# Kernel tuning notes

Hardware: AMD Instinct MI355X
Metric: run time of the kernel (lower is better)

The kernel has to match this reference:

```python
import jax, jax.numpy as jnp
import numpy as np

N_INST, N_PERS, N_PROD = 20000, 50000, 30000
E_INST, E_PERS, E_PROD = 160000, 400000, 240000
F_IN, HID, HEADS, OUT = 128, 64, 4, 2
D = HID * HEADS  # 256
NEG_SLOPE_ATT = 0.2   # GATv2 attention leaky-relu slope
NEG_SLOPE_ACT = 0.01  # F.leaky_relu default
BN_EPS = 1e-5


def gatv2(x, src, dst, Wl, Wr, att, b, N):
    """Single-relation GATv2Conv (concat heads, add_self_loops=True)."""
    loop = jnp.arange(N, dtype=src.dtype)
    s = jnp.concatenate([src, loop])
    d = jnp.concatenate([dst, loop])
    H, C = att.shape
    hl = (x @ Wl).reshape(N, H, C)  # source transform
    hr = (x @ Wr).reshape(N, H, C)  # target transform
    e = jax.nn.leaky_relu(hl[s] + hr[d], NEG_SLOPE_ATT)        # [E,H,C]
    score = jnp.einsum('ehc,hc->eh', e, att)                   # [E,H]
    mx = jax.lax.stop_gradient(jax.ops.segment_max(score, d, num_segments=N))
    ex = jnp.exp(score - mx[d])
    den = jax.ops.segment_sum(ex, d, num_segments=N)           # [N,H]
    alpha = ex / (den[d] + 1e-16)
    out = jax.ops.segment_sum(alpha[..., None] * hl[s], d, num_segments=N)
    return out.reshape(N, H * C) + b


def batchnorm(x, g, b):
    mu = jnp.mean(x, axis=0)
    var = jnp.var(x, axis=0)
    return (x - mu) * jax.lax.rsqrt(var + BN_EPS) * g + b


def setup_inputs() -> dict:
    key = jax.random.key(0)
    ks = jax.random.split(key, 16)
    s = 0.05
    return {
        'x_inst': jax.random.normal(ks[0], (N_INST, F_IN), jnp.float32),
        'x_pers': jax.random.normal(ks[1], (N_PERS, F_IN), jnp.float32),
        'x_prod': jax.random.normal(ks[2], (N_PROD, F_IN), jnp.float32),
        'ei_inst': jax.random.randint(ks[3], (2, E_INST), 0, N_INST, jnp.int32),
        'ei_pers': jax.random.randint(ks[4], (2, E_PERS), 0, N_PERS, jnp.int32),
        'ei_prod': jax.random.randint(ks[5], (2, E_PROD), 0, N_PROD, jnp.int32),
        'Wl1': jax.random.normal(ks[6], (3, F_IN, D), jnp.float32) * s,
        'Wr1': jax.random.normal(ks[7], (3, F_IN, D), jnp.float32) * s,
        'att1': jax.random.normal(ks[8], (3, HEADS, HID), jnp.float32) * s,
        'b1': jnp.zeros((3, D), jnp.float32),
        'Wl2': jax.random.normal(ks[9], (3, D, D), jnp.float32) * s,
        'Wr2': jax.random.normal(ks[10], (3, D, D), jnp.float32) * s,
        'att2': jax.random.normal(ks[11], (3, HEADS, HID), jnp.float32) * s,
        'b2': jnp.zeros((3, D), jnp.float32),
        'bn_g': jnp.ones((3, D), jnp.float32),
        'bn_b': jnp.zeros((3, D), jnp.float32),
        'cW': jax.random.normal(ks[12], (D, OUT), jnp.float32) * s,
        'cb': jnp.zeros((OUT,), jnp.float32),
    }


def reference(x_inst, x_pers, x_prod, ei_inst, ei_pers, ei_prod,
              Wl1, Wr1, att1, b1, Wl2, Wr2, att2, b2,
              bn_g, bn_b, cW, cb):
    xs = (x_inst, x_pers, x_prod)
    eis = (ei_inst, ei_pers, ei_prod)
    outs = []
    for i in range(3):  # fixed set of node types
        x = xs[i]
        N = x.shape[0]
        src, dst = eis[i][0], eis[i][1]
        h = gatv2(x, src, dst, Wl1[i], Wr1[i], att1[i], b1[i], N)
        h = jax.nn.leaky_relu(batchnorm(h, bn_g[i], bn_b[i]), NEG_SLOPE_ACT)
        h = gatv2(h, src, dst, Wl2[i], Wr2[i], att2[i], b2[i], N)
        h = jax.nn.leaky_relu(batchnorm(h, bn_g[i], bn_b[i]), NEG_SLOPE_ACT)
        outs.append(h @ cW + cb)
    return tuple(outs)
```

## Files before the change

### kernel.cpp

```cpp
#include <hip/hip_runtime.h>

#define DFEAT 256
#define NEG_ATT 0.2f
#define NEG_ACT 0.01f
#define BN_EPS 1e-5f

typedef short bf16x8 __attribute__((ext_vector_type(8)));
typedef float f32x4 __attribute__((ext_vector_type(4)));

struct Int3 { int a[3]; };
struct Cp3 { const void* p[3]; };
struct Vp3 { void* p[3]; };

__device__ __forceinline__ float lrelu(float x, float s) { return x > 0.f ? x : s * x; }

__device__ __forceinline__ unsigned short f2bf(float f) {
    union { float f; unsigned int u; } v; v.f = f;
    unsigned int u = v.u;
    unsigned int r = (u + 0x7FFFu + ((u >> 16) & 1u)) >> 16;
    return (unsigned short)r;
}
__device__ __forceinline__ float bf2f(unsigned short s) {
    union { unsigned int u; float f; } v; v.u = ((unsigned int)s) << 16;
    return v.f;
}

__global__ __launch_bounds__(256)
void hist_all_k(Cp3 dst, Int3 E, int* __restrict__ counts_all, Int3 nodeOff) {
    int t = blockIdx.y;
    int e = blockIdx.x * 256 + threadIdx.x;
    if (e >= E.a[t]) return;
    const int* dstp = (const int*)dst.p[t];
    atomicAdd(&counts_all[nodeOff.a[t] + dstp[e]], 1);
}

__global__ __launch_bounds__(256)
void scan1_all_k(const int* __restrict__ counts_all, int* __restrict__ offs_all,
                 int* __restrict__ bsums_all, Int3 N, Int3 nodeOff, Int3 bOff) {
    int t = blockIdx.y;
    if (blockIdx.x * 256 >= N.a[t]) return;
    const int* counts = counts_all + nodeOff.a[t];
    int* offs = offs_all + nodeOff.a[t] + t;
    int* bsums = bsums_all + bOff.a[t];
    __shared__ int buf[256];
    int tt = threadIdx.x;
    int i = blockIdx.x * 256 + tt;
    int v = (i < N.a[t]) ? counts[i] : 0;
    buf[tt] = v;
    __syncthreads();
    for (int off = 1; off < 256; off <<= 1) {
        int x = (tt >= off) ? buf[tt - off] : 0;
        __syncthreads();
        buf[tt] += x;
        __syncthreads();
    }
    if (i < N.a[t]) offs[i] = buf[tt];
    if (tt == 255) bsums[blockIdx.x] = buf[255];
}

__global__ __launch_bounds__(256)
void scan2_all_k(int* __restrict__ bsums_all, Int3 N, Int3 bOff) {
    int t = blockIdx.x;
    int nb = (N.a[t] + 255) / 256;
    int* bsums = bsums_all + bOff.a[t];
    __shared__ int buf[256];
    __shared__ int carry_s;
    int tt = threadIdx.x;
    if (tt == 0) carry_s = 0;
    __syncthreads();
    for (int base = 0; base < nb; base += 256) {
        int i = base + tt;
        int v = (i < nb) ? bsums[i] : 0;
        buf[tt] = v;
        __syncthreads();
        for (int off = 1; off < 256; off <<= 1) {
            int x = (tt >= off) ? buf[tt - off] : 0;
            __syncthreads();
            buf[tt] += x;
            __syncthreads();
        }
        int incl = buf[tt];
        int c = carry_s;
        if (i < nb) bsums[i] = c + incl - v;
        __syncthreads();
        if (tt == 255) carry_s = c + buf[255];
        __syncthreads();
    }
}

__global__ __launch_bounds__(256)
void scan3_all_k(int* __restrict__ offs_all, const int* __restrict__ counts_all,
                 const int* __restrict__ bsums_all, Int3 N, Int3 E,
                 Int3 nodeOff, Int3 bOff) {
    int t = blockIdx.y;
    if (blockIdx.x * 256 >= N.a[t]) return;
    int* offs = offs_all + nodeOff.a[t] + t;
    const int* counts = counts_all + nodeOff.a[t];
    const int* bsums = bsums_all + bOff.a[t];
    int i = blockIdx.x * 256 + threadIdx.x;
    if (i < N.a[t]) offs[i] = offs[i] - counts[i] + bsums[blockIdx.x];
    if (i == 0) offs[N.a[t]] = E.a[t];
}

__global__ __launch_bounds__(256)
void scatter_all_k(Cp3 src, Cp3 dst, Int3 E, const int* __restrict__ offs_all,
                   int* __restrict__ counts_all, int* __restrict__ csr_all,
                   Int3 nodeOff, Int3 edgeOff) {
    int t = blockIdx.y;
    int e = blockIdx.x * 256 + threadIdx.x;
    if (e >= E.a[t]) return;
    const int* srcp = (const int*)src.p[t];
    const int* dstp = (const int*)dst.p[t];
    const int* offs = offs_all + nodeOff.a[t] + t;
    int* cursor = counts_all + nodeOff.a[t];
    int* csr = csr_all + edgeOff.a[t];
    int d = dstp[e];
    int pos = atomicSub(&cursor[d], 1) - 1;
    csr[offs[d] + pos] = srcp[e];
}

__global__ __launch_bounds__(256)
void wcast_all_k(const float* __restrict__ Wl1, const float* __restrict__ Wr1,
                 const float* __restrict__ Wl2, const float* __restrict__ Wr2,
                 unsigned short* __restrict__ Bt1, unsigned short* __restrict__ Bt2) {
    int idx = blockIdx.x * 256 + threadIdx.x;
    const int S1 = 3 * 512 * 128;
    const int S2 = 3 * 512 * 256;
    if (idx < S1) {
        int ty = idx / (512 * 128);
        int r = idx - ty * (512 * 128);
        int n = r >> 7, k = r & 127;
        const float* W = ((n < 256) ? Wl1 : Wr1) + (size_t)ty * 128 * 256;
        Bt1[idx] = f2bf(W[(size_t)k * 256 + (n & 255)]);
    } else if (idx < S1 + S2) {
        int r2 = idx - S1;
        int ty = r2 / (512 * 256);
        int r = r2 - ty * (512 * 256);
        int n = r >> 8, k = r & 255;
        const float* W = ((n < 256) ? Wl2 : Wr2) + (size_t)ty * 256 * 256;
        Bt2[r2] = f2bf(W[(size_t)k * 256 + (n & 255)]);
    }
}

template<int AF32>
__global__ __launch_bounds__(256)
void mfma_gemm_all_k(Cp3 Ap3, Cp3 Bp3, Vp3 Cp3v, Int3 M3, int K) {
    int t = blockIdx.z;
    int M = M3.a[t];
    int bm = blockIdx.x * 128;
    if (bm >= M) return;
    const void* Ap = Ap3.p[t];
    const unsigned short* Bt = (const unsigned short*)Bp3.p[t];
    unsigned short* C = (unsigned short*)Cp3v.p[t];
    const int LDK = 40;
    __shared__ unsigned short As[128 * LDK];
    __shared__ unsigned short Bs[128 * LDK];
    int tid = threadIdx.x;
    int bn = blockIdx.y * 128;
    int wid = tid >> 6, lane = tid & 63;
    int quad = lane >> 4, l16 = lane & 15;
    int mw = (wid & 1) * 64, nw = (wid >> 1) * 64;
    f32x4 acc[4][4] = {};
    for (int k0 = 0; k0 < K; k0 += 32) {
#pragma unroll
        for (int i = 0; i < 2; ++i) {
            int c = tid + 256 * i;
            int row = c >> 2, ko = (c & 3) * 8;
            int ra = bm + row; if (ra >= M) ra = M - 1;
            if (AF32) {
                const float* Af = (const float*)Ap;
                float4 a0 = *(const float4*)(Af + (size_t)ra * K + k0 + ko);
                float4 a1 = *(const float4*)(Af + (size_t)ra * K + k0 + ko + 4);
                ushort4 lo, hi;
                lo.x = f2bf(a0.x); lo.y = f2bf(a0.y); lo.z = f2bf(a0.z); lo.w = f2bf(a0.w);
                hi.x = f2bf(a1.x); hi.y = f2bf(a1.y); hi.z = f2bf(a1.z); hi.w = f2bf(a1.w);
                *(ushort4*)&As[row * LDK + ko] = lo;
                *(ushort4*)&As[row * LDK + ko + 4] = hi;
            } else {
                const unsigned short* Ab = (const unsigned short*)Ap;
                uint4 va = *(const uint4*)(Ab + (size_t)ra * K + k0 + ko);
                *(uint4*)&As[row * LDK + ko] = va;
            }
            uint4 vb = *(const uint4*)(Bt + (size_t)(bn + row) * K + k0 + ko);
            *(uint4*)&Bs[row * LDK + ko] = vb;
        }
        __syncthreads();
        bf16x8 af[4], bfv[4];
#pragma unroll
        for (int i = 0; i < 4; ++i)
            af[i] = *(bf16x8*)&As[(mw + 16 * i + l16) * LDK + quad * 8];
#pragma unroll
        for (int u = 0; u < 4; ++u)
            bfv[u] = *(bf16x8*)&Bs[(nw + 16 * u + l16) * LDK + quad * 8];
#pragma unroll
        for (int i = 0; i < 4; ++i)
#pragma unroll
            for (int u = 0; u < 4; ++u)
                acc[i][u] = __builtin_amdgcn_mfma_f32_16x16x32_bf16(af[i], bfv[u], acc[i][u], 0, 0, 0);
        __syncthreads();
    }
#pragma unroll
    for (int i = 0; i < 4; ++i) {
#pragma unroll
        for (int r = 0; r < 4; ++r) {
            int grow = bm + mw + 16 * i + quad * 4 + r;
            if (grow < M) {
#pragma unroll
                for (int u = 0; u < 4; ++u) {
                    int gcol = bn + nw + 16 * u + l16;
                    C[(size_t)grow * 512 + gcol] = f2bf(acc[i][u][r]);
                }
            }
        }
    }
}

__global__ __launch_bounds__(256)
void gat_gather_all_k(Cp3 hl3, Cp3 offs3, Cp3 csr3, Cp3 att3, Cp3 bias3,
                      Vp3 out3, Int3 N3) {
    int t = blockIdx.z;
    int N = N3.a[t];
    int wave = (blockIdx.x * 256 + threadIdx.x) >> 6;
    int lane = threadIdx.x & 63;
    if (wave >= N) return;
    const unsigned short* hl = (const unsigned short*)hl3.p[t];
    const unsigned short* hr = hl + 256;
    const int* offs = (const int*)offs3.p[t];
    const int* csr = (const int*)csr3.p[t];
    const float* att = (const float*)att3.p[t];
    const float* bias = (const float*)bias3.p[t];
    unsigned short* out = (unsigned short*)out3.p[t];
    int d = wave;
    int f4 = lane << 2;
    ushort4 hru = *(const ushort4*)(hr + (size_t)d * 512 + f4);
    float hr0 = bf2f(hru.x), hr1 = bf2f(hru.y), hr2 = bf2f(hru.z), hr3 = bf2f(hru.w);
    float4 av  = *(const float4*)(att + f4);
    float4 bv  = *(const float4*)(bias + f4);
    float l = 0.f, ac0 = 0.f, ac1 = 0.f, ac2 = 0.f, ac3 = 0.f;

    auto update = [&](ushort4 u) {
        float h0 = bf2f(u.x), h1 = bf2f(u.y), h2 = bf2f(u.z), h3 = bf2f(u.w);
        float e0 = lrelu(h0 + hr0, NEG_ATT);
        float e1 = lrelu(h1 + hr1, NEG_ATT);
        float e2 = lrelu(h2 + hr2, NEG_ATT);
        float e3 = lrelu(h3 + hr3, NEG_ATT);
        float part = e0 * av.x + e1 * av.y + e2 * av.z + e3 * av.w;
        part += __shfl_xor(part, 1, 16);
        part += __shfl_xor(part, 2, 16);
        part += __shfl_xor(part, 4, 16);
        part += __shfl_xor(part, 8, 16);
        float p = __expf(part);
        l += p;
        ac0 += p * h0; ac1 += p * h1; ac2 += p * h2; ac3 += p * h3;
    };

    update(*(const ushort4*)(hl + (size_t)d * 512 + f4));

    int beg = offs[d], end = offs[d + 1];
    int deg = end - beg;
    for (int base = 0; base < deg; base += 64) {
        int cnt = min(64, deg - base);
        int my = (base + lane < deg) ? csr[beg + base + lane] : d;
        for (int j = 0; j < cnt; j += 8) {
            int kk = min(8, cnt - j);
            ushort4 v[8];
#pragma unroll
            for (int u = 0; u < 8; ++u) {
                int s = __shfl(my, (j + u) & 63);
                if (u < kk) v[u] = *(const ushort4*)(hl + (size_t)s * 512 + f4);
            }
#pragma unroll
            for (int u = 0; u < 8; ++u)
                if (u < kk) update(v[u]);
        }
    }
    float inv = 1.f / (l + 1e-16f);
    ushort4 o;
    o.x = f2bf(ac0 * inv + bv.x);
    o.y = f2bf(ac1 * inv + bv.y);
    o.z = f2bf(ac2 * inv + bv.z);
    o.w = f2bf(ac3 * inv + bv.w);
    *(ushort4*)(out + (size_t)d * DFEAT + f4) = o;
}

__global__ __launch_bounds__(256)
void bn_stats_all_k(Cp3 h3, Vp3 st3, Int3 N3) {
    int t = blockIdx.y;
    const unsigned short* hp = (const unsigned short*)h3.p[t];
    float* st = (float*)st3.p[t];
    long total = (long)N3.a[t] * 256;
    int tid = threadIdx.x;
    long gt = (long)blockIdx.x * 256 + tid;
    long stride = (long)gridDim.x * 256 * 8;
    float s[8] = {0.f}, s2[8] = {0.f};
    for (long p = gt * 8; p < total; p += stride) {
        uint4 u = *(const uint4*)(hp + p);
        unsigned short* us = (unsigned short*)&u;
#pragma unroll
        for (int j = 0; j < 8; ++j) { float v = bf2f(us[j]); s[j] += v; s2[j] += v * v; }
    }
#pragma unroll
    for (int j = 0; j < 8; ++j) { s[j] += __shfl_xor(s[j], 32); s2[j] += __shfl_xor(s2[j], 32); }
    __shared__ float lds[2048];
    int wv = tid >> 6, lane = tid & 63;
    if (lane < 32) {
#pragma unroll
        for (int j = 0; j < 8; ++j) {
            lds[wv * 512 + lane * 8 + j] = s[j];
            lds[wv * 512 + 256 + lane * 8 + j] = s2[j];
        }
    }
    __syncthreads();
    for (int q = tid; q < 512; q += 256) {
        float v = lds[q] + lds[512 + q] + lds[1024 + q] + lds[1536 + q];
        atomicAdd(&st[q], v);
    }
}

__global__ __launch_bounds__(256)
void bn_apply_all_k(Vp3 h3, Cp3 st3, const float* __restrict__ gb, const float* __restrict__ bb,
                    Int3 N3) {
    int t = blockIdx.y;
    int N = N3.a[t];
    size_t idx = (size_t)blockIdx.x * 256 + threadIdx.x;
    if (idx >= (size_t)N * 64) return;
    unsigned short* h = (unsigned short*)h3.p[t];
    const float* stats = (const float*)st3.p[t];
    const float* g = gb + (size_t)t * DFEAT;
    const float* b = bb + (size_t)t * DFEAT;
    int f4 = ((int)(idx & 63)) << 2;
    float invN = 1.f / (float)N;
    ushort4 u = ((const ushort4*)h)[idx];
    float vv[4] = {bf2f(u.x), bf2f(u.y), bf2f(u.z), bf2f(u.w)};
    ushort4 ov;
    unsigned short* op = (unsigned short*)&ov;
#pragma unroll
    for (int j = 0; j < 4; ++j) {
        int f = f4 + j;
        float mu  = stats[f] * invN;
        float var = stats[DFEAT + f] * invN - mu * mu;
        float sc  = g[f] / sqrtf(var + BN_EPS);
        float val = (vv[j] - mu) * sc + b[f];
        op[j] = f2bf(lrelu(val, NEG_ACT));
    }
    ((ushort4*)h)[idx] = ov;
}

__global__ __launch_bounds__(256)
void bn_cls_all_k(Cp3 R3, Cp3 st3, const float* __restrict__ gb, const float* __restrict__ bb,
                  const float* __restrict__ cW, const float* __restrict__ cb,
                  Vp3 out3, Int3 N3) {
    int t = blockIdx.y;
    int N = N3.a[t];
    int wave = (blockIdx.x * 256 + threadIdx.x) >> 6;
    int lane = threadIdx.x & 63;
    if (wave >= N) return;
    const unsigned short* R = (const unsigned short*)R3.p[t];
    const float* stats = (const float*)st3.p[t];
    const float* g = gb + (size_t)t * DFEAT;
    const float* b = bb + (size_t)t * DFEAT;
    float* out = (float*)out3.p[t];
    int f4 = lane << 2;
    float invN = 1.f / (float)N;
    ushort4 u = *(const ushort4*)(R + (size_t)wave * DFEAT + f4);
    float vv[4] = {bf2f(u.x), bf2f(u.y), bf2f(u.z), bf2f(u.w)};
    float p0 = 0.f, p1 = 0.f;
#pragma unroll
    for (int j = 0; j < 4; ++j) {
        int f = f4 + j;
        float mu  = stats[f] * invN;
        float var = stats[DFEAT + f] * invN - mu * mu;
        float sc  = g[f] / sqrtf(var + BN_EPS);
        float val = lrelu((vv[j] - mu) * sc + b[f], NEG_ACT);
        float2 w = *(const float2*)(cW + (size_t)f * 2);
        p0 += val * w.x;
        p1 += val * w.y;
    }
#pragma unroll
    for (int off = 1; off < 64; off <<= 1) {
        p0 += __shfl_xor(p0, off);
        p1 += __shfl_xor(p1, off);
    }
    if (lane == 0) {
        out[(size_t)wave * 2 + 0] = p0 + cb[0];
        out[(size_t)wave * 2 + 1] = p1 + cb[1];
    }
}

extern "C" void kernel_launch(void* const* d_in, const int* in_sizes, int n_in,
                              void* d_out, int out_size, void* d_ws, size_t ws_size,
                              hipStream_t stream) {
    const float* x0 = (const float*)d_in[0];
    const float* x1 = (const float*)d_in[1];
    const float* x2 = (const float*)d_in[2];
    const int* ei[3] = {(const int*)d_in[3], (const int*)d_in[4], (const int*)d_in[5]};
    const float* Wl1 = (const float*)d_in[6];
    const float* Wr1 = (const float*)d_in[7];
    const float* att1 = (const float*)d_in[8];
    const float* b1 = (const float*)d_in[9];
    const float* Wl2 = (const float*)d_in[10];
    const float* Wr2 = (const float*)d_in[11];
    const float* att2 = (const float*)d_in[12];
    const float* b2 = (const float*)d_in[13];
    const float* bn_g = (const float*)d_in[14];
    const float* bn_b = (const float*)d_in[15];
    const float* cW = (const float*)d_in[16];
    const float* cb = (const float*)d_in[17];

    Int3 N3, E3, nodeOff, edgeOff, bOff;
    N3.a[0] = in_sizes[0] / 128; N3.a[1] = in_sizes[1] / 128; N3.a[2] = in_sizes[2] / 128;
    E3.a[0] = in_sizes[3] / 2;   E3.a[1] = in_sizes[4] / 2;   E3.a[2] = in_sizes[5] / 2;
    int Ntot = 0, Etot = 0, btot = 0;
    int maxN = 0, maxE = 0;
    for (int i = 0; i < 3; ++i) {
        nodeOff.a[i] = Ntot; edgeOff.a[i] = Etot; bOff.a[i] = btot;
        Ntot += N3.a[i]; Etot += E3.a[i]; btot += (N3.a[i] + 255) / 256;
        if (N3.a[i] > maxN) maxN = N3.a[i];
        if (E3.a[i] > maxE) maxE = E3.a[i];
    }

    char* w = (char*)d_ws;
    auto alloc_b = [&](size_t bytes) -> void* {
        void* p = (void*)w;
        w += (bytes + 255) & ~(size_t)255;
        return p;
    };
    unsigned short* C_all  = (unsigned short*)alloc_b((size_t)Ntot * 512 * sizeof(unsigned short));
    unsigned short* Rb_all = (unsigned short*)alloc_b((size_t)Ntot * DFEAT * sizeof(unsigned short));
    unsigned short* Bt1 = (unsigned short*)alloc_b((size_t)3 * 512 * 128 * sizeof(unsigned short));
    unsigned short* Bt2 = (unsigned short*)alloc_b((size_t)3 * 512 * 256 * sizeof(unsigned short));
    int* counts_all = (int*)alloc_b((size_t)Ntot * sizeof(int));
    int* offs_all   = (int*)alloc_b((size_t)(Ntot + 3) * sizeof(int));
    int* csr_all    = (int*)alloc_b((size_t)Etot * sizeof(int));
    int* bsums_all  = (int*)alloc_b((size_t)btot * sizeof(int));
    float* stats_all = (float*)alloc_b((size_t)6 * 512 * sizeof(float));

    Cp3 srcP, dstP, xP, Bt1P, Bt2P, hlP, offsP, csrP, att1P, att2P, b1P, b2P;
    Cp3 RbCP, st1CP, st2CP;
    Vp3 CP, RbP, st1P, st2P, outP;
    for (int i = 0; i < 3; ++i) {
        srcP.p[i] = ei[i];
        dstP.p[i] = ei[i] + E3.a[i];
        xP.p[i] = (i == 0) ? (const void*)x0 : (i == 1) ? (const void*)x1 : (const void*)x2;
        Bt1P.p[i] = Bt1 + (size_t)i * 512 * 128;
        Bt2P.p[i] = Bt2 + (size_t)i * 512 * 256;
        CP.p[i] = C_all + (size_t)nodeOff.a[i] * 512;
        hlP.p[i] = CP.p[i];
        RbP.p[i] = Rb_all + (size_t)nodeOff.a[i] * DFEAT;
        RbCP.p[i] = RbP.p[i];
        offsP.p[i] = offs_all + nodeOff.a[i] + i;
        csrP.p[i] = csr_all + edgeOff.a[i];
        att1P.p[i] = att1 + (size_t)i * DFEAT;
        att2P.p[i] = att2 + (size_t)i * DFEAT;
        b1P.p[i] = b1 + (size_t)i * DFEAT;
        b2P.p[i] = b2 + (size_t)i * DFEAT;
        st1P.p[i] = stats_all + (size_t)i * 512;
        st2P.p[i] = stats_all + (size_t)(3 + i) * 512;
        st1CP.p[i] = st1P.p[i];
        st2CP.p[i] = st2P.p[i];
        outP.p[i] = (float*)d_out + (size_t)nodeOff.a[i] * 2;
    }

    int maxNblk = (maxN + 255) / 256;
    int maxEblk = (maxE + 255) / 256;
    int maxMtile = (maxN + 127) / 128;
    int maxNwave = (maxN + 3) / 4;

    hipMemsetAsync(counts_all, 0, (size_t)Ntot * sizeof(int), stream);
    hipMemsetAsync(stats_all, 0, (size_t)6 * 512 * sizeof(float), stream);
    {
        int tot = 3 * 512 * 128 + 3 * 512 * 256;
        wcast_all_k<<<(tot + 255) / 256, 256, 0, stream>>>(Wl1, Wr1, Wl2, Wr2, Bt1, Bt2);
    }

    hist_all_k<<<dim3(maxEblk, 3), 256, 0, stream>>>(dstP, E3, counts_all, nodeOff);
    scan1_all_k<<<dim3(maxNblk, 3), 256, 0, stream>>>(counts_all, offs_all, bsums_all, N3, nodeOff, bOff);
    scan2_all_k<<<3, 256, 0, stream>>>(bsums_all, N3, bOff);
    scan3_all_k<<<dim3(maxNblk, 3), 256, 0, stream>>>(offs_all, counts_all, bsums_all, N3, E3, nodeOff, bOff);
    scatter_all_k<<<dim3(maxEblk, 3), 256, 0, stream>>>(srcP, dstP, E3, offs_all, counts_all, csr_all, nodeOff, edgeOff);

    mfma_gemm_all_k<1><<<dim3(maxMtile, 4, 3), 256, 0, stream>>>(xP, Bt1P, CP, N3, 128);
    gat_gather_all_k<<<dim3(maxNwave, 1, 3), 256, 0, stream>>>(hlP, offsP, csrP, att1P, b1P, RbP, N3);
    bn_stats_all_k<<<dim3(512, 3), 256, 0, stream>>>(RbCP, st1P, N3);
    bn_apply_all_k<<<dim3(maxNwave, 3), 256, 0, stream>>>(RbP, st1CP, bn_g, bn_b, N3);

    mfma_gemm_all_k<0><<<dim3(maxMtile, 4, 3), 256, 0, stream>>>(RbCP, Bt2P, CP, N3, 256);
    gat_gather_all_k<<<dim3(maxNwave, 1, 3), 256, 0, stream>>>(hlP, offsP, csrP, att2P, b2P, RbP, N3);
    bn_stats_all_k<<<dim3(512, 3), 256, 0, stream>>>(RbCP, st2P, N3);

    bn_cls_all_k<<<dim3(maxNwave, 3), 256, 0, stream>>>(RbCP, st2CP, bn_g, bn_b, cW, cb, outP, N3);
}
```

Measured before the change: 581.2 us.

## Process four edges per wave in GATv2 gather with 16 features per lane

The gather kernel now splits each wave into four quads of 16 lanes. Each quad handles a different edge, and each lane holds 16 features loaded through two 16-byte loads instead of one 8-byte load. Per-head score reduction needs only two shuffles, and a cross-quad reduction of the accumulators and denominator happens once at the end. This is meant to raise memory-level parallelism and cut shuffle overhead per edge. In exchange it uses more registers per lane and adds a final 34-shuffle reduction.

```diff
diff --git a/kernel.cpp b/kernel.cpp
--- a/kernel.cpp
+++ b/kernel.cpp
@@ -23,6 +23,12 @@
 __device__ __forceinline__ float bf2f(unsigned short s) {
     union { unsigned int u; float f; } v; v.u = ((unsigned int)s) << 16;
     return v.f;
+}
+__device__ __forceinline__ float u_lo(unsigned u) {
+    union { unsigned u; float f; } v; v.u = u << 16; return v.f;
+}
+__device__ __forceinline__ float u_hi(unsigned u) {
+    union { unsigned u; float f; } v; v.u = u & 0xffff0000u; return v.f;
 }
 
 __global__ __launch_bounds__(256)
@@ -223,64 +229,105 @@
     int wave = (blockIdx.x * 256 + threadIdx.x) >> 6;
     int lane = threadIdx.x & 63;
     if (wave >= N) return;
-    const unsigned short* hl = (const unsigned short*)hl3.p[t];
-    const unsigned short* hr = hl + 256;
+    int d = wave;
+    int quad = lane >> 4, l16 = lane & 15;
+    const char* hlB = (const char*)hl3.p[t];
     const int* offs = (const int*)offs3.p[t];
     const int* csr = (const int*)csr3.p[t];
     const float* att = (const float*)att3.p[t];
     const float* bias = (const float*)bias3.p[t];
     unsigned short* out = (unsigned short*)out3.p[t];
-    int d = wave;
-    int f4 = lane << 2;
-    ushort4 hru = *(const ushort4*)(hr + (size_t)d * 512 + f4);
-    float hr0 = bf2f(hru.x), hr1 = bf2f(hru.y), hr2 = bf2f(hru.z), hr3 = bf2f(hru.w);
-    float4 av  = *(const float4*)(att + f4);
-    float4 bv  = *(const float4*)(bias + f4);
-    float l = 0.f, ac0 = 0.f, ac1 = 0.f, ac2 = 0.f, ac3 = 0.f;
-
-    auto update = [&](ushort4 u) {
-        float h0 = bf2f(u.x), h1 = bf2f(u.y), h2 = bf2f(u.z), h3 = bf2f(u.w);
-        float e0 = lrelu(h0 + hr0, NEG_ATT);
-        float e1 = lrelu(h1 + hr1, NEG_ATT);
-        float e2 = lrelu(h2 + hr2, NEG_ATT);
-        float e3 = lrelu(h3 + hr3, NEG_ATT);
-        float part = e0 * av.x + e1 * av.y + e2 * av.z + e3 * av.w;
-        part += __shfl_xor(part, 1, 16);
-        part += __shfl_xor(part, 2, 16);
-        part += __shfl_xor(part, 4, 16);
-        part += __shfl_xor(part, 8, 16);
-        float p = __expf(part);
-        l += p;
-        ac0 += p * h0; ac1 += p * h1; ac2 += p * h2; ac3 += p * h3;
+
+    unsigned fOff = (unsigned)(l16 << 5);
+
+    float hrf[16], attf[16], ac[16];
+    {
+        unsigned off = ((unsigned)d << 10) + 512u + fOff;
+        uint4 u0 = *(const uint4*)(hlB + off);
+        uint4 u1 = *(const uint4*)(hlB + off + 16);
+        const unsigned* up0 = (const unsigned*)&u0;
+        const unsigned* up1 = (const unsigned*)&u1;
+#pragma unroll
+        for (int j = 0; j < 4; ++j) {
+            hrf[2 * j] = u_lo(up0[j]);     hrf[2 * j + 1] = u_hi(up0[j]);
+            hrf[8 + 2 * j] = u_lo(up1[j]); hrf[8 + 2 * j + 1] = u_hi(up1[j]);
+        }
+        const float4* ap4 = (const float4*)(att + (l16 << 4));
+#pragma unroll
+        for (int j = 0; j < 4; ++j) {
+            float4 v = ap4[j];
+            attf[4 * j] = v.x; attf[4 * j + 1] = v.y;
+            attf[4 * j + 2] = v.z; attf[4 * j + 3] = v.w;
+        }
+    }
+#pragma unroll
+    for (int j = 0; j < 16; ++j) ac[j] = 0.f;
+    float lsum = 0.f;
+
+    auto edge_update = [&](int s, bool active) {
+        unsigned off = ((unsigned)s << 10) + fOff;
+        uint4 u0 = *(const uint4*)(hlB + off);
+        uint4 u1 = *(const uint4*)(hlB + off + 16);
+        const unsigned* up0 = (const unsigned*)&u0;
+        const unsigned* up1 = (const unsigned*)&u1;
+        float h[16];
+#pragma unroll
+        for (int j = 0; j < 4; ++j) {
+            h[2 * j] = u_lo(up0[j]);     h[2 * j + 1] = u_hi(up0[j]);
+            h[8 + 2 * j] = u_lo(up1[j]); h[8 + 2 * j + 1] = u_hi(up1[j]);
+        }
+        float part = 0.f;
+#pragma unroll
+        for (int j = 0; j < 16; ++j) {
+            float x = h[j] + hrf[j];
+            x = fmaxf(x, NEG_ATT * x);
+            part = fmaf(x, attf[j], part);
+        }
+        part += __shfl_xor(part, 1);
+        part += __shfl_xor(part, 2);
+        float p = active ? __expf(part) : 0.f;
+        lsum += p;
+#pragma unroll
+        for (int j = 0; j < 16; ++j) ac[j] = fmaf(p, h[j], ac[j]);
     };
 
-    update(*(const ushort4*)(hl + (size_t)d * 512 + f4));
-
-    int beg = offs[d], end = offs[d + 1];
-    int deg = end - beg;
+    if (quad == 0) edge_update(d, true);
+
+    int beg = offs[d];
+    int deg = offs[d + 1] - beg;
     for (int base = 0; base < deg; base += 64) {
         int cnt = min(64, deg - base);
         int my = (base + lane < deg) ? csr[beg + base + lane] : d;
-        for (int j = 0; j < cnt; j += 8) {
-            int kk = min(8, cnt - j);
-            ushort4 v[8];
-#pragma unroll
-            for (int u = 0; u < 8; ++u) {
-                int s = __shfl(my, (j + u) & 63);
-                if (u < kk) v[u] = *(const ushort4*)(hl + (size_t)s * 512 + f4);
-            }
-#pragma unroll
-            for (int u = 0; u < 8; ++u)
-                if (u < kk) update(v[u]);
-        }
-    }
-    float inv = 1.f / (l + 1e-16f);
-    ushort4 o;
-    o.x = f2bf(ac0 * inv + bv.x);
-    o.y = f2bf(ac1 * inv + bv.y);
-    o.z = f2bf(ac2 * inv + bv.z);
-    o.w = f2bf(ac3 * inv + bv.w);
-    *(ushort4*)(out + (size_t)d * DFEAT + f4) = o;
+#pragma unroll 4
+        for (int g = 0; g < cnt; g += 4) {
+            int vi = g + quad;
+            int s = __shfl(my, vi);
+            edge_update(s, vi < cnt);
+        }
+    }
+
+    lsum += __shfl_xor(lsum, 16);
+    lsum += __shfl_xor(lsum, 32);
+#pragma unroll
+    for (int j = 0; j < 16; ++j) {
+        ac[j] += __shfl_xor(ac[j], 16);
+        ac[j] += __shfl_xor(ac[j], 32);
+    }
+
+    if (quad == 0) {
+        float inv = 1.f / (lsum + 1e-16f);
+        const float* bp = bias + (l16 << 4);
+        unsigned o[8];
+#pragma unroll
+        for (int j = 0; j < 8; ++j) {
+            float v0 = ac[2 * j] * inv + bp[2 * j];
+            float v1 = ac[2 * j + 1] * inv + bp[2 * j + 1];
+            o[j] = (unsigned)f2bf(v0) | ((unsigned)f2bf(v1) << 16);
+        }
+        unsigned short* op = out + ((size_t)d << 8) + (l16 << 4);
+        *(uint4*)op = make_uint4(o[0], o[1], o[2], o[3]);
+        *(uint4*)(op + 8) = make_uint4(o[4], o[5], o[6], o[7]);
+    }
 }
 
 __global__ __launch_bounds__(256)
```

Result: slower. 694.8 us (+19.5%).
